# Performance work log

Hardware: AMD Instinct MI355X
Metric: run time of the kernel (lower is better)

The kernel has to match this reference:

```python
import jax, jax.numpy as jnp
import numpy as np

B, L, D, H, DK, DV = 16, 1024, 512, 8, 64, 64
FACTOR = 1
TOP_K = int(FACTOR * np.log(L))  # 6, static


def autocorrelation(q, k, v, top_k):
    # q, k, v: [B, L, H, E] (Autoformer layout)
    Bs, Ls, Hs, Es = q.shape
    qp = jnp.transpose(q, (0, 2, 3, 1))  # [B,H,E,L]
    kp = jnp.transpose(k, (0, 2, 3, 1))
    vp = jnp.transpose(v, (0, 2, 3, 1))
    qf = jnp.fft.rfft(qp, axis=-1)
    kf = jnp.fft.rfft(kp, axis=-1)
    corr = jnp.fft.irfft(qf * jnp.conj(kf), n=Ls, axis=-1)  # [B,H,E,L]
    # time_delay_agg_training: average corr over heads and channels
    mean_value = corr.mean(axis=(1, 2))  # [B,L]
    _, index = jax.lax.top_k(mean_value.mean(axis=0), top_k)  # [top_k] shared delays
    weights = jnp.take(mean_value, index, axis=1)  # [B,top_k]
    tmp_corr = jax.nn.softmax(weights, axis=-1)  # [B,top_k]
    # roll(v, -delay) gathered for all top_k delays at once
    idx = (index[:, None] + jnp.arange(Ls)[None, :]) % Ls  # [top_k, L]
    patterns = vp[..., idx]  # [B,H,E,top_k,L]
    agg = jnp.einsum('bhekl,bk->bhel', patterns, tmp_corr)  # [B,H,E,L]
    return jnp.transpose(agg, (0, 3, 1, 2))  # [B,L,H,E]


def setup_inputs() -> dict:
    key = jax.random.key(0)
    ks = jax.random.split(key, 7)
    Q = jax.random.normal(ks[0], (B, L, D), jnp.float32)
    K = jax.random.normal(ks[1], (B, L, D), jnp.float32)
    V = jax.random.normal(ks[2], (B, L, D), jnp.float32)
    attn_mask = jnp.zeros((B, 1, L, L), jnp.bool_)  # ignored by AutoCorrelation
    s = 0.02
    WQ = jax.random.normal(ks[3], (D, H * DK), jnp.float32) * s
    WK = jax.random.normal(ks[4], (D, H * DK), jnp.float32) * s
    WV = jax.random.normal(ks[5], (D, H * DV), jnp.float32) * s
    Wfc = jax.random.normal(ks[6], (H * DV, D), jnp.float32) * s
    return {"Q": Q, "K": K, "V": V, "attn_mask": attn_mask,
            "WQ": WQ, "WK": WK, "WV": WV, "Wfc": Wfc}


def reference(Q, K, V, attn_mask, WQ, WK, WV, Wfc):
    del attn_mask  # full AutoCorrelation ignores the mask
    q_s = (Q @ WQ).reshape(B, L, H, DK)  # [B,L,H,dk]
    k_s = (K @ WK).reshape(B, L, H, DK)
    v_s = (V @ WV).reshape(B, L, H, DV)
    out = autocorrelation(q_s, k_s, v_s, TOP_K)  # [B,L,H,dv]
    context = out.reshape(B, L, H * DV)
    return context @ Wfc  # [B,L,D]
```

## Files before the change

kernel.cpp:

```cpp
#include <hip/hip_runtime.h>
#include <math.h>

namespace {

constexpr int Bb = 16;
constexpr int Ll = 1024;
constexpr int Dd = 512;
constexpr int TOPK = 6;
constexpr int Kc = 512;
constexpr int NT = Kc / 32;

typedef short  short8 __attribute__((ext_vector_type(8)));
typedef float  f32x4  __attribute__((ext_vector_type(4)));

__device__ __forceinline__ short f2bf(float x) {
  unsigned u = __builtin_bit_cast(unsigned, x);
  u += 0x7fffu + ((u >> 16) & 1u);
  return (short)(u >> 16);
}
__device__ __forceinline__ float bf2f(short b) {
  unsigned u = ((unsigned)(unsigned short)b) << 16;
  return __builtin_bit_cast(float, u);
}
__device__ __forceinline__ void g2l16(const void* g, void* l) {
  __builtin_amdgcn_global_load_lds(
      (const __attribute__((address_space(1))) unsigned*)g,
      (__attribute__((address_space(3))) unsigned*)l, 16, 0, 0);
}
__device__ __forceinline__ short8 cvt8(float4 a, float4 b) {
  short8 o;
  o[0] = f2bf(a.x); o[1] = f2bf(a.y); o[2] = f2bf(a.z); o[3] = f2bf(a.w);
  o[4] = f2bf(b.x); o[5] = f2bf(b.y); o[6] = f2bf(b.z); o[7] = f2bf(b.w);
  return o;
}

#define BARRIER() do { asm volatile("" ::: "memory"); \
    __builtin_amdgcn_s_barrier(); \
    asm volatile("" ::: "memory"); } while (0)
#define VMCNT3() asm volatile("s_waitcnt vmcnt(3)" ::: "memory")
#define VMCNT1() asm volatile("s_waitcnt vmcnt(1)" ::: "memory")
#define VMCNT0() asm volatile("s_waitcnt vmcnt(0)" ::: "memory")
#define LGKM0()  do { asm volatile("s_waitcnt lgkmcnt(0)" ::: "memory"); \
    __builtin_amdgcn_sched_barrier(0); } while (0)

template<int MODE>
__global__ __launch_bounds__(512) void gemm_ring(
    const void* __restrict__ Aq, const void* __restrict__ Ak,
    const void* __restrict__ Av,
    const short* __restrict__ Bq, const short* __restrict__ Bk,
    const short* __restrict__ Bv,
    void* __restrict__ Cq, void* __restrict__ Ck, void* __restrict__ Cv)
{
  __shared__ short lds3[3][12288];
  __shared__ float bins[384];

  const int tid = threadIdx.x;
  const int z   = blockIdx.z;

  int m0, n0;
  if (MODE == 1) {
    const int fb = blockIdx.x;
    const int s  = (fb & 7) * 4 + (fb >> 3);
    m0 = (s >> 3) * 256;  n0 = (s & 7) * 128;
  } else {
    const int fb = blockIdx.x;
    const int s  = (fb & 7) * 32 + (fb >> 3);
    m0 = (s >> 2) * 256;  n0 = (s & 3) * 128;
  }

  const float* Af = nullptr;
  const short* Ab = nullptr;
  const short* Bp;
  if (MODE == 0) {
    Af = (const float*)((z == 0) ? Aq : (z == 1) ? Ak : Av);
    Bp = (z == 0) ? Bq : (z == 1) ? Bk : Bv;
  } else if (MODE == 1) {
    Ab = (const short*)Aq + (size_t)z * Ll * Kc;
    Bp = Bq + (size_t)z * Ll * Kc;
  } else {
    Ab = (const short*)Aq;
    Bp = Bq;
  }

  const int rB  = tid >> 2;
  const int c8B = (tid & 3) ^ ((rB >> 1) & 3);
  const short* gB = Bp + (size_t)(n0 + rB) * Kc + c8B * 8;
  const int destB = 8192 + tid * 8;

  const int rA  = tid >> 2;
  const int c8A = (tid & 3) ^ ((rA >> 1) & 3);
  const short* gA0 = nullptr; const short* gA1 = nullptr;
  if (MODE != 0) {
    gA0 = Ab + (size_t)(m0 + rA) * Kc + c8A * 8;
    gA1 = gA0 + (size_t)128 * Kc;
  }
  const int destA0 = tid * 8, destA1 = tid * 8 + 4096;

  const int rP  = tid >> 1;
  const int c8P = 2 * (tid & 1);
  const float* gAf = nullptr;
  int uW0 = 0, uW1 = 0;
  if (MODE == 0) {
    gAf = Af + (size_t)(m0 + rP) * Kc + c8P * 8;
    uW0 = rP * 4 + (c8P ^ ((rP >> 1) & 3));
    uW1 = uW0 ^ 1;
  }

  const int lane = tid & 63;
  const int wid  = tid >> 6;
  const int wr = wid >> 1, wn = wid & 1;
  const int lo = lane & 15, hi = lane >> 4;
  int aoff[4], boff[4];
#pragma unroll
  for (int i = 0; i < 4; ++i) {
    const int ar = wr * 64 + i * 16 + lo;
    aoff[i] = (ar * 4 + (hi ^ ((ar >> 1) & 3))) * 8;
  }
#pragma unroll
  for (int j = 0; j < 4; ++j) {
    const int br = wn * 64 + j * 16 + lo;
    boff[j] = 8192 + (br * 4 + (hi ^ ((br >> 1) & 3))) * 8;
  }

  if (MODE == 1 && tid < 384) bins[tid] = 0.f;

  f32x4 acc[4][4];
#pragma unroll
  for (int i = 0; i < 4; ++i)
#pragma unroll
    for (int j = 0; j < 4; ++j) acc[i][j] = (f32x4){0.f, 0.f, 0.f, 0.f};

  if (MODE == 0) {
    float4 p0 = *(const float4*)(gAf + 0);
    float4 p1 = *(const float4*)(gAf + 4);
    float4 p2 = *(const float4*)(gAf + 8);
    float4 p3 = *(const float4*)(gAf + 12);
    g2l16(gB, &lds3[0][destB]);
    float4 q0 = *(const float4*)(gAf + 32);
    float4 q1 = *(const float4*)(gAf + 36);
    float4 q2 = *(const float4*)(gAf + 40);
    float4 q3 = *(const float4*)(gAf + 44);
    g2l16(gB + 32, &lds3[1][destB]);
    *(short8*)&lds3[0][uW0 * 8] = cvt8(p0, p1);
    *(short8*)&lds3[0][uW1 * 8] = cvt8(p2, p3);
    *(short8*)&lds3[1][uW0 * 8] = cvt8(q0, q1);
    *(short8*)&lds3[1][uW1 * 8] = cvt8(q2, q3);
    LGKM0();
    VMCNT1();
  } else {
    g2l16(gA0,      &lds3[0][destA0]);
    g2l16(gA1,      &lds3[0][destA1]);
    g2l16(gB,       &lds3[0][destB]);
    g2l16(gA0 + 32, &lds3[1][destA0]);
    g2l16(gA1 + 32, &lds3[1][destA1]);
    g2l16(gB  + 32, &lds3[1][destB]);
    VMCNT3();
  }
  BARRIER();

  int sr = 0, sw = 2;
#pragma unroll 1
  for (int t = 0; t < NT; ++t) {
    const short* L = &lds3[sr][0];
    short8 af[4], bfr[4];
#pragma unroll
    for (int i = 0; i < 4; ++i) af[i]  = *(const short8*)(L + aoff[i]);
#pragma unroll
    for (int j = 0; j < 4; ++j) bfr[j] = *(const short8*)(L + boff[j]);

    float4 s0, s1, s2, s3;
    if (t < NT - 2) {
      const int ke = (t + 2) * 32;
      if (MODE == 0) {
        s0 = *(const float4*)(gAf + ke + 0);
        s1 = *(const float4*)(gAf + ke + 4);
        s2 = *(const float4*)(gAf + ke + 8);
        s3 = *(const float4*)(gAf + ke + 12);
        g2l16(gB + ke, &lds3[sw][destB]);
      } else {
        g2l16(gA0 + ke, &lds3[sw][destA0]);
        g2l16(gA1 + ke, &lds3[sw][destA1]);
        g2l16(gB  + ke, &lds3[sw][destB]);
      }
    }

    BARRIER();
    __builtin_amdgcn_s_setprio(1);
#pragma unroll
    for (int i = 0; i < 4; ++i)
#pragma unroll
      for (int j = 0; j < 4; ++j)
        acc[i][j] = __builtin_amdgcn_mfma_f32_16x16x32_bf16(af[i], bfr[j], acc[i][j], 0, 0, 0);
    __builtin_amdgcn_s_setprio(0);

    if (MODE == 0) {
      if (t < NT - 2) {
        *(short8*)&lds3[sw][uW0 * 8] = cvt8(s0, s1);
        *(short8*)&lds3[sw][uW1 * 8] = cvt8(s2, s3);
        LGKM0();
        VMCNT1();
      } else if (t == NT - 2) {
        VMCNT0();
      }
    } else {
      if (t < NT - 2)       VMCNT3();
      else if (t == NT - 2) VMCNT0();
    }
    BARRIER();
    sr = (sr == 2) ? 0 : sr + 1;
    sw = (sw == 2) ? 0 : sw + 1;
  }

  if (MODE == 0) {
    short* C = (short*)((z == 0) ? Cq : (z == 1) ? Ck : Cv);
#pragma unroll
    for (int i = 0; i < 4; ++i)
#pragma unroll
      for (int r = 0; r < 4; ++r) {
        const size_t row = m0 + wr * 64 + i * 16 + hi * 4 + r;
#pragma unroll
        for (int j = 0; j < 4; ++j)
          C[row * Dd + n0 + wn * 64 + j * 16 + lo] = f2bf(acc[i][j][r]);
      }
  } else if (MODE == 2) {
    float* C = (float*)Cq;
#pragma unroll
    for (int i = 0; i < 4; ++i)
#pragma unroll
      for (int r = 0; r < 4; ++r) {
        const size_t row = m0 + wr * 64 + i * 16 + hi * 4 + r;
#pragma unroll
        for (int j = 0; j < 4; ++j)
          C[row * Dd + n0 + wn * 64 + j * 16 + lo] = acc[i][j][r];
      }
  } else {
    float red[7][4];
#pragma unroll
    for (int d = 0; d < 7; ++d)
#pragma unroll
      for (int r = 0; r < 4; ++r) red[d][r] = 0.f;
#pragma unroll
    for (int i = 0; i < 4; ++i)
#pragma unroll
      for (int j = 0; j < 4; ++j)
#pragma unroll
        for (int r = 0; r < 4; ++r) red[i - j + 3][r] += acc[i][j][r];

    const int dbase = 127 + (wr * 64 - wn * 64) + 4 * hi - lo;
#pragma unroll
    for (int d = 0; d < 7; ++d)
#pragma unroll
      for (int r = 0; r < 4; ++r)
        atomicAdd(&bins[dbase + 16 * (d - 3) + r], red[d][r]);
    __syncthreads();
    if (tid < 383) {
      float* mv = (float*)Cq;
      const int l = (m0 - n0 + tid - 127) & (Ll - 1);
      atomicAdd(&mv[z * Ll + l], bins[tid]);
    }
  }
}

__global__ __launch_bounds__(256) void wtrans(
    const float* __restrict__ w0, const float* __restrict__ w1,
    const float* __restrict__ w2, const float* __restrict__ w3,
    short* __restrict__ o0, short* __restrict__ o1,
    short* __restrict__ o2, short* __restrict__ o3)
{
  const int z = blockIdx.z;
  const float* W = (z == 0) ? w0 : (z == 1) ? w1 : (z == 2) ? w2 : w3;
  short* O = (z == 0) ? o0 : (z == 1) ? o1 : (z == 2) ? o2 : o3;
  __shared__ float t[32][33];
  const int tx = threadIdx.x & 31, ty = threadIdx.x >> 5;
  const int bx = blockIdx.x, by = blockIdx.y;
#pragma unroll
  for (int s = 0; s < 32; s += 8)
    t[ty + s][tx] = W[(size_t)(by * 32 + ty + s) * 512 + bx * 32 + tx];
  __syncthreads();
#pragma unroll
  for (int s = 0; s < 32; s += 8)
    O[(size_t)(bx * 32 + ty + s) * 512 + by * 32 + tx] = f2bf(t[tx][ty + s]);
}

__global__ void zero_mv(float* __restrict__ mv)
{
  int i = blockIdx.x * 256 + threadIdx.x;
  if (i < Bb * Ll) mv[i] = 0.f;
}

__global__ __launch_bounds__(1024) void topk_softmax(
    const float* __restrict__ mean_value,
    int* __restrict__ idx_out, float* __restrict__ w_out)
{
  __shared__ float vals[1024];
  __shared__ int   inds[1024];
  __shared__ float bm[1024];
  __shared__ int   topi[TOPK];
  const int t = threadIdx.x;
  float s = 0.f;
  for (int b = 0; b < Bb; ++b) s += mean_value[b * Ll + t];
  bm[t] = s;
  __syncthreads();
  for (int k = 0; k < TOPK; ++k) {
    bool taken = false;
    for (int j = 0; j < k; ++j) taken |= (topi[j] == t);
    vals[t] = taken ? -INFINITY : bm[t];
    inds[t] = t;
    __syncthreads();
    for (int stride = 512; stride > 0; stride >>= 1) {
      if (t < stride) {
        if (vals[t + stride] > vals[t]) { vals[t] = vals[t + stride]; inds[t] = inds[t + stride]; }
      }
      __syncthreads();
    }
    if (t == 0) topi[k] = inds[0];
    __syncthreads();
  }
  if (t < TOPK) idx_out[t] = topi[t];
  if (t < Bb) {
    float wv[TOPK], mx = -INFINITY;
#pragma unroll
    for (int k = 0; k < TOPK; ++k) {
      wv[k] = mean_value[t * Ll + topi[k]] * (1.f / 512.f);
      mx = fmaxf(mx, wv[k]);
    }
    float sum = 0.f;
#pragma unroll
    for (int k = 0; k < TOPK; ++k) { wv[k] = expf(wv[k] - mx); sum += wv[k]; }
#pragma unroll
    for (int k = 0; k < TOPK; ++k) w_out[t * TOPK + k] = wv[k] / sum;
  }
}

__global__ __launch_bounds__(256) void aggregate(
    const short* __restrict__ vs, const float* __restrict__ w,
    const int* __restrict__ idx, short* __restrict__ ctx)
{
  const int b = blockIdx.y;
  __shared__ float ww[8];
  __shared__ int   ii[8];
  if (threadIdx.x < TOPK) { ww[threadIdx.x] = w[b * TOPK + threadIdx.x]; ii[threadIdx.x] = idx[threadIdx.x]; }
  __syncthreads();
  const int l = blockIdx.x * 4 + (threadIdx.x >> 6);
  const int c = (threadIdx.x & 63) * 8;
  const short* vb = vs + (size_t)b * Ll * Dd;
  float a[8] = {};
#pragma unroll
  for (int k = 0; k < TOPK; ++k) {
    const short8 vv = *(const short8*)&vb[(size_t)((l + ii[k]) & (Ll - 1)) * Dd + c];
    const float wk = ww[k];
#pragma unroll
    for (int e = 0; e < 8; ++e) a[e] = fmaf(wk, bf2f(vv[e]), a[e]);
  }
  short8 o;
#pragma unroll
  for (int e = 0; e < 8; ++e) o[e] = f2bf(a[e]);
  *(short8*)&ctx[((size_t)b * Ll + l) * Dd + c] = o;
}

}

extern "C" void kernel_launch(void* const* d_in, const int* in_sizes, int n_in,
                              void* d_out, int out_size, void* d_ws, size_t ws_size,
                              hipStream_t stream)
{
  const float* Q   = (const float*)d_in[0];
  const float* K   = (const float*)d_in[1];
  const float* V   = (const float*)d_in[2];
  const float* WQ  = (const float*)d_in[4];
  const float* WK  = (const float*)d_in[5];
  const float* WV  = (const float*)d_in[6];
  const float* Wfc = (const float*)d_in[7];
  float* out = (float*)d_out;

  char* ws = (char*)d_ws;
  const size_t SB = (size_t)Bb * Ll * Dd * sizeof(short);
  short* qsb  = (short*)(ws);
  short* ksb  = (short*)(ws + 1 * SB);
  short* vsb  = (short*)(ws + 2 * SB);
  short* ctxb = (short*)(ws + 3 * SB);
  short* wtq  = (short*)(ws + 4 * SB);
  short* wtk  = wtq + 512 * 512;
  short* wtv  = wtk + 512 * 512;
  short* wtf  = wtv + 512 * 512;
  float* mv   = (float*)(wtf + 512 * 512);
  float* w    = mv + Bb * Ll;
  int*   idx  = (int*)(w + 128);

  wtrans<<<dim3(16, 16, 4), 256, 0, stream>>>(WQ, WK, WV, Wfc, wtq, wtk, wtv, wtf);
  zero_mv<<<64, 256, 0, stream>>>(mv);

  gemm_ring<0><<<dim3(256, 1, 3), 512, 0, stream>>>(
      Q, K, V, wtq, wtk, wtv, qsb, ksb, vsb);
  gemm_ring<1><<<dim3(32, 1, 16), 512, 0, stream>>>(
      qsb, nullptr, nullptr, ksb, nullptr, nullptr, mv, nullptr, nullptr);
  topk_softmax<<<1, 1024, 0, stream>>>(mv, idx, w);
  aggregate<<<dim3(Ll / 4, Bb), 256, 0, stream>>>(vsb, w, idx, ctxb);
  gemm_ring<2><<<dim3(256, 1, 1), 512, 0, stream>>>(
      ctxb, nullptr, nullptr, wtf, nullptr, nullptr, out, nullptr, nullptr);
}
```

Baseline: 159.0 us.

## Fold WQ·WKᵀ into a Gram matrix and skip the K projection

The correlation sum over channels, q·k, equals Q·(WQ WKᵀ)·Kᵀ. A small GEMM now precomputes G = WQ·WKᵀ, Q is projected through G, and raw K is only converted to bf16 by an elementwise path. This removes one full 512x512 projection GEMM over B*L rows. It also stages the GEMM epilogues through LDS so global stores are wide and coalesced, and merges the weight-prep and zeroing kernels. The trade-off is more bf16 rounding from the folded weights, and an extra small GEMM launch.

```diff
diff --git a/kernel.cpp b/kernel.cpp
--- a/kernel.cpp
+++ b/kernel.cpp
@@ -57,23 +57,39 @@
   const int tid = threadIdx.x;
   const int z   = blockIdx.z;
 
+  if (MODE == 0 && z == 2) {
+    const float* src = (const float*)Av;
+    short* dst = (short*)Cv;
+    const int base = blockIdx.x * 512 + tid;
+#pragma unroll
+    for (int it = 0; it < 8; ++it) {
+      const size_t li = (size_t)(base + it * 131072) * 8;
+      const float4 a = *(const float4*)(src + li);
+      const float4 b = *(const float4*)(src + li + 4);
+      *(short8*)&dst[li] = cvt8(a, b);
+    }
+    return;
+  }
+
   int m0, n0;
-  if (MODE == 1) {
+  {
     const int fb = blockIdx.x;
-    const int s  = (fb & 7) * 4 + (fb >> 3);
-    m0 = (s >> 3) * 256;  n0 = (s & 7) * 128;
-  } else {
-    const int fb = blockIdx.x;
-    const int s  = (fb & 7) * 32 + (fb >> 3);
-    m0 = (s >> 2) * 256;  n0 = (s & 3) * 128;
+    if (MODE == 1) {
+      const int s = (fb & 7) * 4 + (fb >> 3);
+      m0 = (s >> 3) * 256;  n0 = (s & 7) * 128;
+    } else {
+      const int chunk = gridDim.x >> 3;
+      const int s = (fb & 7) * chunk + (fb >> 3);
+      m0 = (s >> 2) * 256;  n0 = (s & 3) * 128;
+    }
   }
 
   const float* Af = nullptr;
   const short* Ab = nullptr;
   const short* Bp;
   if (MODE == 0) {
-    Af = (const float*)((z == 0) ? Aq : (z == 1) ? Ak : Av);
-    Bp = (z == 0) ? Bq : (z == 1) ? Bk : Bv;
+    Af = (const float*)((z == 0) ? Aq : Ak);
+    Bp = (z == 0) ? Bq : Bk;
   } else if (MODE == 1) {
     Ab = (const short*)Aq + (size_t)z * Ll * Kc;
     Bp = Bq + (size_t)z * Ll * Kc;
@@ -212,27 +228,40 @@
   }
 
   if (MODE == 0) {
-    short* C = (short*)((z == 0) ? Cq : (z == 1) ? Ck : Cv);
+    short* eb = ((short*)lds3) + wid * 4608;
+    short* C = (short*)((z == 0) ? Cq : Ck);
 #pragma unroll
     for (int i = 0; i < 4; ++i)
 #pragma unroll
-      for (int r = 0; r < 4; ++r) {
-        const size_t row = m0 + wr * 64 + i * 16 + hi * 4 + r;
+      for (int r = 0; r < 4; ++r)
 #pragma unroll
         for (int j = 0; j < 4; ++j)
-          C[row * Dd + n0 + wn * 64 + j * 16 + lo] = f2bf(acc[i][j][r]);
+          eb[(i * 16 + hi * 4 + r) * 72 + j * 16 + lo] = f2bf(acc[i][j][r]);
+#pragma unroll
+    for (int p = 0; p < 8; ++p) {
+      const short8 v = *(const short8*)&eb[(p * 8 + (lane >> 3)) * 72 + (lane & 7) * 8];
+      *(short8*)&C[(size_t)(m0 + wr * 64 + p * 8 + (lane >> 3)) * Dd
+                   + n0 + wn * 64 + (lane & 7) * 8] = v;
+    }
+  } else if (MODE == 2) {
+    float* fbuf = ((float*)lds3) + wid * 2176;
+    float* C = (float*)Cq;
+#pragma unroll
+    for (int p = 0; p < 2; ++p) {
+#pragma unroll
+      for (int ii = 0; ii < 2; ++ii)
+#pragma unroll
+        for (int r = 0; r < 4; ++r)
+#pragma unroll
+          for (int j = 0; j < 4; ++j)
+            fbuf[(ii * 16 + hi * 4 + r) * 68 + j * 16 + lo] = acc[2 * p + ii][j][r];
+#pragma unroll
+      for (int q = 0; q < 8; ++q) {
+        const float4 v = *(const float4*)&fbuf[(q * 4 + (lane >> 4)) * 68 + (lane & 15) * 4];
+        *(float4*)&C[(size_t)(m0 + wr * 64 + p * 32 + q * 4 + (lane >> 4)) * Dd
+                     + n0 + wn * 64 + (lane & 15) * 4] = v;
       }
-  } else if (MODE == 2) {
-    float* C = (float*)Cq;
-#pragma unroll
-    for (int i = 0; i < 4; ++i)
-#pragma unroll
-      for (int r = 0; r < 4; ++r) {
-        const size_t row = m0 + wr * 64 + i * 16 + hi * 4 + r;
-#pragma unroll
-        for (int j = 0; j < 4; ++j)
-          C[row * Dd + n0 + wn * 64 + j * 16 + lo] = acc[i][j][r];
-      }
+    }
   } else {
     float red[7][4];
 #pragma unroll
@@ -261,31 +290,35 @@
   }
 }
 
-__global__ __launch_bounds__(256) void wtrans(
-    const float* __restrict__ w0, const float* __restrict__ w1,
-    const float* __restrict__ w2, const float* __restrict__ w3,
-    short* __restrict__ o0, short* __restrict__ o1,
-    short* __restrict__ o2, short* __restrict__ o3)
+__global__ __launch_bounds__(256) void prep(
+    const float* __restrict__ WQ, const float* __restrict__ WV,
+    const float* __restrict__ Wfc,
+    short* __restrict__ wqb, short* __restrict__ wtv,
+    short* __restrict__ wtf, float* __restrict__ mv)
 {
+  __shared__ float t[32][33];
   const int z = blockIdx.z;
-  const float* W = (z == 0) ? w0 : (z == 1) ? w1 : (z == 2) ? w2 : w3;
-  short* O = (z == 0) ? o0 : (z == 1) ? o1 : (z == 2) ? o2 : o3;
-  __shared__ float t[32][33];
   const int tx = threadIdx.x & 31, ty = threadIdx.x >> 5;
   const int bx = blockIdx.x, by = blockIdx.y;
-#pragma unroll
-  for (int s = 0; s < 32; s += 8)
-    t[ty + s][tx] = W[(size_t)(by * 32 + ty + s) * 512 + bx * 32 + tx];
-  __syncthreads();
-#pragma unroll
-  for (int s = 0; s < 32; s += 8)
-    O[(size_t)(bx * 32 + ty + s) * 512 + by * 32 + tx] = f2bf(t[tx][ty + s]);
-}
-
-__global__ void zero_mv(float* __restrict__ mv)
-{
-  int i = blockIdx.x * 256 + threadIdx.x;
-  if (i < Bb * Ll) mv[i] = 0.f;
+  if (z == 0) {
+#pragma unroll
+    for (int s = 0; s < 32; s += 8) {
+      const size_t o = (size_t)(by * 32 + ty + s) * 512 + bx * 32 + tx;
+      wqb[o] = f2bf(WQ[o]);
+    }
+    const int fb = by * 16 + bx;
+    if (threadIdx.x < 64) mv[fb * 64 + threadIdx.x] = 0.f;
+  } else {
+    const float* W = (z == 1) ? WV : Wfc;
+    short* O = (z == 1) ? wtv : wtf;
+#pragma unroll
+    for (int s = 0; s < 32; s += 8)
+      t[ty + s][tx] = W[(size_t)(by * 32 + ty + s) * 512 + bx * 32 + tx];
+    __syncthreads();
+#pragma unroll
+    for (int s = 0; s < 32; s += 8)
+      O[(size_t)(bx * 32 + ty + s) * 512 + by * 32 + tx] = f2bf(t[tx][ty + s]);
+  }
 }
 
 __global__ __launch_bounds__(1024) void topk_softmax(
@@ -375,27 +408,32 @@
 
   char* ws = (char*)d_ws;
   const size_t SB = (size_t)Bb * Ll * Dd * sizeof(short);
-  short* qsb  = (short*)(ws);
-  short* ksb  = (short*)(ws + 1 * SB);
-  short* vsb  = (short*)(ws + 2 * SB);
+  short* qg   = (short*)(ws);
+  short* vsb  = (short*)(ws + 1 * SB);
+  short* kb   = (short*)(ws + 2 * SB);
   short* ctxb = (short*)(ws + 3 * SB);
-  short* wtq  = (short*)(ws + 4 * SB);
-  short* wtk  = wtq + 512 * 512;
-  short* wtv  = wtk + 512 * 512;
+  short* wqb  = (short*)(ws + 4 * SB);
+  short* wtv  = wqb + 512 * 512;
   short* wtf  = wtv + 512 * 512;
-  float* mv   = (float*)(wtf + 512 * 512);
+  short* Gt   = wtf + 512 * 512;
+  float* mv   = (float*)(Gt + 512 * 512);
   float* w    = mv + Bb * Ll;
   int*   idx  = (int*)(w + 128);
 
-  wtrans<<<dim3(16, 16, 4), 256, 0, stream>>>(WQ, WK, WV, Wfc, wtq, wtk, wtv, wtf);
-  zero_mv<<<64, 256, 0, stream>>>(mv);
+  prep<<<dim3(16, 16, 3), 256, 0, stream>>>(WQ, WV, Wfc, wqb, wtv, wtf, mv);
+
+  gemm_ring<0><<<dim3(8, 1, 1), 512, 0, stream>>>(
+      WK, nullptr, nullptr, wqb, nullptr, nullptr, Gt, nullptr, nullptr);
 
   gemm_ring<0><<<dim3(256, 1, 3), 512, 0, stream>>>(
-      Q, K, V, wtq, wtk, wtv, qsb, ksb, vsb);
+      Q, V, K, Gt, wtv, nullptr, qg, vsb, kb);
+
   gemm_ring<1><<<dim3(32, 1, 16), 512, 0, stream>>>(
-      qsb, nullptr, nullptr, ksb, nullptr, nullptr, mv, nullptr, nullptr);
+      qg, nullptr, nullptr, kb, nullptr, nullptr, mv, nullptr, nullptr);
+
   topk_softmax<<<1, 1024, 0, stream>>>(mv, idx, w);
   aggregate<<<dim3(Ll / 4, Bb), 256, 0, stream>>>(vsb, w, idx, ctxb);
+
   gemm_ring<2><<<dim3(256, 1, 1), 512, 0, stream>>>(
       ctxb, nullptr, nullptr, wtf, nullptr, nullptr, out, nullptr, nullptr);
 }
```

New measurement: 179.1 us. +12.7%, slower.
